# Performance work log

Measured on AMD Instinct MI355X. Metric: run time of the kernel, lower is better.

The kernel has to match this reference:

```python
import jax, jax.numpy as jnp
import numpy as np

M, NM, EM = 7, 1024, 32768        # modules, nodes/module, edges/module
N, E = M * NM, M * EM
F, D, H = 128, 64, 4              # node feats, hidden_channels, heads
HC = H * D


def setup_inputs() -> dict:
    key = jax.random.key(0)
    ks = jax.random.split(key, 20)
    x = jax.random.normal(ks[0], (N, F), jnp.float32)
    # intra-module edges; nodes of module m occupy [m*NM, (m+1)*NM)
    base = jnp.repeat(jnp.arange(M, dtype=jnp.int32) * NM, EM)
    src = base + jax.random.randint(ks[1], (E,), 0, NM, dtype=jnp.int32)
    dst = base + jax.random.randint(ks[2], (E,), 0, NM, dtype=jnp.int32)
    edge_index = jnp.stack([src, dst])
    module_assignments = jnp.repeat(jnp.arange(M, dtype=jnp.int32), NM)
    rn = lambda k, sh: jax.random.normal(k, sh, jnp.float32) * 0.05
    return dict(
        x=x, edge_index=edge_index, module_assignments=module_assignments,
        g1_w=rn(ks[3], (M, F, H, D)), g1_as=rn(ks[4], (M, H, D)), g1_ad=rn(ks[5], (M, H, D)),
        g1_b=jnp.zeros((M, HC), jnp.float32),
        g2_w=rn(ks[6], (M, HC, 1, D)), g2_as=rn(ks[7], (M, 1, D)), g2_ad=rn(ks[8], (M, 1, D)),
        g2_b=jnp.zeros((M, D), jnp.float32),
        sa_in_w=rn(ks[9], (M, 3 * D, D)), sa_in_b=jnp.zeros((M, 3 * D), jnp.float32),
        sa_out_w=rn(ks[10], (M, D, D)), sa_out_b=jnp.zeros((M, D), jnp.float32),
        ca_in_w=rn(ks[11], (3 * D, D)), ca_in_b=jnp.zeros((3 * D,), jnp.float32),
        ca_out_w=rn(ks[12], (D, D)), ca_out_b=jnp.zeros((D,), jnp.float32),
        fusion_w=jnp.ones((M,), jnp.float32) / M,
        fc_w=rn(ks[13], (M * D, D)), fc_b=jnp.zeros((D,), jnp.float32),
        c1_w=rn(ks[14], (D, D // 2)), c1_b=jnp.zeros((D // 2,), jnp.float32),
        c2_w=rn(ks[15], (D // 2, 2)), c2_b=jnp.zeros((2,), jnp.float32))


def _gat(x, src, dst, W, a_s, a_d, b, concat):
    # PyG-style GATConv (eval mode, add_self_loops=True). x:[NM,Fin], W:[Fin,h,c]
    h = jnp.einsum('nf,fhc->nhc', x, W)          # [NM,h,c]
    es = (h * a_s).sum(-1)                        # [NM,h]
    ed = (h * a_d).sum(-1)
    sl = jnp.arange(NM, dtype=src.dtype)
    s = jnp.concatenate([src, sl])                # add self-loops
    d = jnp.concatenate([dst, sl])
    e = jax.nn.leaky_relu(es[s] + ed[d], 0.2)     # [E+NM,h]
    mx = jax.ops.segment_max(e, d, num_segments=NM)
    ex = jnp.exp(e - mx[d])
    den = jax.ops.segment_sum(ex, d, num_segments=NM)
    alpha = ex / (den[d] + 1e-16)
    out = jax.ops.segment_sum(alpha[:, :, None] * h[s], d, num_segments=NM)  # [NM,h,c]
    out = out.reshape(NM, -1) if concat else out.mean(axis=1)
    return out + b


def _mha(x, in_w, in_b, out_w, out_b, nh):
    # torch nn.MultiheadAttention, batch_first, batch=1, eval mode
    L, d = x.shape
    dh = d // nh
    q, k, v = jnp.split(x @ in_w.T + in_b, 3, axis=-1)
    q = q.reshape(L, nh, dh); k = k.reshape(L, nh, dh); v = v.reshape(L, nh, dh)
    att = jax.nn.softmax(jnp.einsum('qhd,khd->hqk', q, k) * (1.0 / np.sqrt(dh)), axis=-1)
    o = jnp.einsum('hqk,khd->qhd', att, v).reshape(L, d)
    return o @ out_w.T + out_b


def _forward(x, edge_index, g1_w, g1_as, g1_ad, g1_b, g2_w, g2_as, g2_ad, g2_b,
             sa_in_w, sa_in_b, sa_out_w, sa_out_b, ca_in_w, ca_in_b, ca_out_w, ca_out_b,
             fusion_w, fc_w, fc_b, c1_w, c1_b, c2_w, c2_b):
    # per-module subgraph extraction + reindex: modules are contiguous node
    # blocks and edges are grouped per module, so mask/relabel is a reshape.
    ei = edge_index.reshape(2, M, EM)
    offs = (jnp.arange(M, dtype=ei.dtype) * NM)[:, None]
    src = ei[0] - offs                 # [M,EM] local indices
    dst = ei[1] - offs
    xm = x.reshape(M, NM, F)

    def per_module(xm_, s_, d_, g1w, g1a, g1d, g1b_, g2w_, g2a, g2d, g2b_, siw, sib, sow, sob):
        h = jax.nn.relu(_gat(xm_, s_, d_, g1w, g1a, g1d, g1b_, True))   # [NM,HC]
        h = jax.nn.relu(_gat(h, s_, d_, g2w_, g2a, g2d, g2b_, False))   # [NM,D]
        h = _mha(h, siw, sib, sow, sob, H)                              # module self-attention
        return h.mean(axis=0)                                            # [D]

    reps = jax.vmap(per_module)(xm, src, dst, g1_w, g1_as, g1_ad, g1_b,
                                g2_w, g2_as, g2_ad, g2_b,
                                sa_in_w, sa_in_b, sa_out_w, sa_out_b)    # [M,D]
    cross = _mha(reps, ca_in_w, ca_in_b, ca_out_w, ca_out_b, H)          # [M,D]
    w = jax.nn.softmax(fusion_w)
    fused = (cross * w[:, None]).reshape(1, M * D) @ fc_w + fc_b         # [1,D]
    out = jax.nn.relu(fused @ c1_w + c1_b) @ c2_w + c2_b                 # [1,2]
    return out, reps


def reference(x, edge_index, module_assignments, g1_w, g1_as, g1_ad, g1_b,
              g2_w, g2_as, g2_ad, g2_b, sa_in_w, sa_in_b, sa_out_w, sa_out_b,
              ca_in_w, ca_in_b, ca_out_w, ca_out_b, fusion_w, fc_w, fc_b,
              c1_w, c1_b, c2_w, c2_b):
    del module_assignments  # encoded as contiguous blocks of NM nodes per module
    return _forward(x, edge_index, g1_w, g1_as, g1_ad, g1_b, g2_w, g2_as, g2_ad, g2_b,
                    sa_in_w, sa_in_b, sa_out_w, sa_out_b, ca_in_w, ca_in_b, ca_out_w,
                    ca_out_b, fusion_w, fc_w, fc_b, c1_w, c1_b, c2_w, c2_b)
```

## Files before the change

### kernel.cpp

```cpp
#include <hip/hip_runtime.h>
#include <hip/hip_bf16.h>
#include <stdint.h>

#define MODS 7
#define NMOD 1024
#define EMOD 32768
#define NN (MODS*NMOD)
#define EE (MODS*EMOD)
#define KC2 4
#define G1B (MODS*16*4)

typedef __hip_bfloat16 bf16;

static __device__ __forceinline__ float lrelu(float x){ return x > 0.f ? x : 0.2f*x; }
static __device__ __forceinline__ float bfu(unsigned short u){ return __uint_as_float(((unsigned)u) << 16); }
static __device__ __forceinline__ float2 f2fma(float2 a, float2 b, float2 c){
  return make_float2(fmaf(a.x,b.x,c.x), fmaf(a.y,b.y,c.y));
}

template<int K, int JT, bool TB, int RT, bool OBF, int SC>
__device__ __forceinline__ void gemm_body(int b, const float* __restrict__ A,
    const float* __restrict__ B, const float* __restrict__ bias, void* __restrict__ Cv,
    const float* __restrict__ a_s, const float* __restrict__ a_d,
    float* __restrict__ es, float* __restrict__ ed) {
  constexpr int jt = JT/64;
  constexpr int rtiles = NMOD/RT;
  constexpr int RPT = RT/16;
  int ct = b % jt; b /= jt;
  int rt = b % rtiles; b /= rtiles;
  int m = b;
  int row0 = m*NMOD + rt*RT;
  int col0 = ct*64;
  __shared__ float Ast[32][RT+4];
  __shared__ float Bs[32][68];
  float acc[RPT][4] = {};
  int tid = threadIdx.x;
  int tr = (tid >> 4) * RPT;
  int tc = (tid & 15) * 4;
  const float* Bm = B + (size_t)m*K*JT;
  for (int k0 = 0; k0 < K; k0 += 32) {
    if constexpr (RT >= 32) {
      constexpr int ANUM = RT*32/1024;
      #pragma unroll
      for (int i = 0; i < ANUM; ++i) {
        int it = tid + i*256;
        int rr = it >> 3, kk0 = (it & 7)*4;
        float4 t = *(const float4*)&A[(size_t)(row0+rr)*K + k0 + kk0];
        Ast[kk0+0][rr] = t.x; Ast[kk0+1][rr] = t.y; Ast[kk0+2][rr] = t.z; Ast[kk0+3][rr] = t.w;
      }
    } else {
      if (tid < 128) {
        int rr = tid >> 3, kk0 = (tid & 7)*4;
        float4 t = *(const float4*)&A[(size_t)(row0+rr)*K + k0 + kk0];
        Ast[kk0+0][rr] = t.x; Ast[kk0+1][rr] = t.y; Ast[kk0+2][rr] = t.z; Ast[kk0+3][rr] = t.w;
      }
    }
    #pragma unroll
    for (int i = 0; i < 2; ++i) {
      int it = tid + i*256;
      if (!TB) {
        int kk = it >> 4, jj0 = (it & 15)*4;
        float4 t = *(const float4*)&Bm[(size_t)(k0+kk)*JT + col0 + jj0];
        Bs[kk][jj0] = t.x; Bs[kk][jj0+1] = t.y; Bs[kk][jj0+2] = t.z; Bs[kk][jj0+3] = t.w;
      } else {
        int jj = it >> 3, kk0 = (it & 7)*4;
        float4 t = *(const float4*)&Bm[(size_t)(col0+jj)*K + k0 + kk0];
        Bs[kk0+0][jj] = t.x; Bs[kk0+1][jj] = t.y; Bs[kk0+2][jj] = t.z; Bs[kk0+3][jj] = t.w;
      }
    }
    __syncthreads();
    #pragma unroll
    for (int kk = 0; kk < 32; ++kk) {
      float4 bv = *(const float4*)&Bs[kk][tc];
      float av[RPT];
      if constexpr (RPT == 4) {
        float4 t = *(const float4*)&Ast[kk][tr];
        av[0] = t.x; av[1] = t.y; av[2] = t.z; av[3] = t.w;
      } else if constexpr (RPT == 2) {
        av[0] = Ast[kk][tr]; av[1] = Ast[kk][tr+1];
      } else {
        av[0] = Ast[kk][tr];
      }
      #pragma unroll
      for (int i = 0; i < RPT; ++i) {
        acc[i][0] += av[i]*bv.x; acc[i][1] += av[i]*bv.y;
        acc[i][2] += av[i]*bv.z; acc[i][3] += av[i]*bv.w;
      }
    }
    __syncthreads();
  }
  float4 bb = {0,0,0,0};
  if (bias) bb = *(const float4*)&bias[m*JT + col0 + tc];
  #pragma unroll
  for (int i = 0; i < RPT; ++i) {
    float4 o = { acc[i][0]+bb.x, acc[i][1]+bb.y, acc[i][2]+bb.z, acc[i][3]+bb.w };
    size_t idx = (size_t)(row0+tr+i)*JT + col0 + tc;
    if constexpr (OBF) {
      bf16* Cp = (bf16*)Cv;
      bf16 tmp[4] = { __float2bfloat16(o.x), __float2bfloat16(o.y),
                      __float2bfloat16(o.z), __float2bfloat16(o.w) };
      *(uint2*)&Cp[idx] = *(const uint2*)tmp;
    } else {
      float* Cp = (float*)Cv;
      *(float4*)&Cp[idx] = o;
    }
  }
  if constexpr (SC == 4) {
    int hh = ct;
    float4 as4 = *(const float4*)&a_s[(m*4 + hh)*64 + tc];
    float4 ad4 = *(const float4*)&a_d[(m*4 + hh)*64 + tc];
    #pragma unroll
    for (int i = 0; i < RPT; ++i) {
      float s = acc[i][0]*as4.x + acc[i][1]*as4.y + acc[i][2]*as4.z + acc[i][3]*as4.w;
      float d = acc[i][0]*ad4.x + acc[i][1]*ad4.y + acc[i][2]*ad4.z + acc[i][3]*ad4.w;
      #pragma unroll
      for (int off = 1; off < 16; off <<= 1) { s += __shfl_xor(s, off); d += __shfl_xor(d, off); }
      if ((tid & 15) == 0) {
        es[(row0+tr+i)*4 + hh] = s;
        ed[(row0+tr+i)*4 + hh] = d;
      }
    }
  }
  if constexpr (SC == 1) {
    float4 as4 = *(const float4*)&a_s[m*64 + tc];
    float4 ad4 = *(const float4*)&a_d[m*64 + tc];
    float s = acc[0][0]*as4.x + acc[0][1]*as4.y + acc[0][2]*as4.z + acc[0][3]*as4.w;
    float d = acc[0][0]*ad4.x + acc[0][1]*ad4.y + acc[0][2]*ad4.z + acc[0][3]*ad4.w;
    #pragma unroll
    for (int off = 1; off < 16; off <<= 1) { s += __shfl_xor(s, off); d += __shfl_xor(d, off); }
    if ((tid & 15) == 0) { es[row0+tr] = s; ed[row0+tr] = d; }
  }
}

__device__ __forceinline__ void hist_body(int mm, const int* __restrict__ dst,
                                          int* __restrict__ rs, int* __restrict__ rs2) {
  __shared__ int hc[NMOD];
  __shared__ int hws[4];
  int tid = threadIdx.x;
  hc[tid] = 0; hc[tid+256] = 0; hc[tid+512] = 0; hc[tid+768] = 0;
  __syncthreads();
  const int4* d4 = (const int4*)(dst + mm*EMOD);
  int base = mm*NMOD;
  for (int it = tid; it < EMOD/4; it += 256) {
    int4 d = d4[it];
    atomicAdd(&hc[d.x - base], 1); atomicAdd(&hc[d.y - base], 1);
    atomicAdd(&hc[d.z - base], 1); atomicAdd(&hc[d.w - base], 1);
  }
  __syncthreads();
  int lane = tid & 63, wid = tid >> 6;
  int i0 = tid*4;
  int v0 = hc[i0], v1 = hc[i0+1], v2 = hc[i0+2], v3 = hc[i0+3];
  int T = v0+v1+v2+v3;
  int X = T;
  #pragma unroll
  for (int off = 1; off < 64; off <<= 1) { int t = __shfl_up(X, off); if (lane >= off) X += t; }
  if (lane == 63) hws[wid] = X;
  __syncthreads();
  int woff = 0;
  #pragma unroll
  for (int w = 0; w < 4; ++w) if (w < wid) woff += hws[w];
  int ex = mm*EMOD + woff + X - T;
  int4 o = make_int4(ex, ex+v0, ex+v0+v1, ex+v0+v1+v2);
  *(int4*)&rs[base + i0]  = o;
  *(int4*)&rs2[base + i0] = o;
  if (mm == MODS-1 && tid == 255) rs[NN] = EE;
}

__global__ __launch_bounds__(256) void k_g1h(const float* __restrict__ x,
    const float* __restrict__ g1w, bf16* __restrict__ h1,
    const float* __restrict__ a_s, const float* __restrict__ a_d,
    float* __restrict__ es, float* __restrict__ ed,
    const int* __restrict__ dst, int* __restrict__ rs, int* __restrict__ rs2) {
  if (blockIdx.x < G1B)
    gemm_body<128,256,false,64,true,4>(blockIdx.x, x, g1w, nullptr, h1, a_s, a_d, es, ed);
  else
    hist_body(blockIdx.x - G1B, dst, rs, rs2);
}

__global__ __launch_bounds__(256) void k_g2s(const float* __restrict__ A,
    const float* __restrict__ B, bf16* __restrict__ h2,
    const float* __restrict__ a_s, const float* __restrict__ a_d,
    float* __restrict__ es, float* __restrict__ ed) {
  gemm_body<256,64,false,16,true,1>(blockIdx.x, A, B, nullptr, h2, a_s, a_d, es, ed);
}

__global__ __launch_bounds__(256) void k_gqkv(const float* __restrict__ A,
    const float* __restrict__ B, const float* __restrict__ bias, float* __restrict__ C) {
  gemm_body<64,192,true,64,false,0>(blockIdx.x, A, B, bias, C, nullptr, nullptr, nullptr, nullptr);
}

__global__ void k_fill(const int* __restrict__ src, const int* __restrict__ dst,
                       int* __restrict__ rs2, int* __restrict__ csr_src) {
  int e = blockIdx.x*256 + threadIdx.x;
  if (e < EE) {
    int pos = atomicAdd(&rs2[dst[e]], 1);
    csr_src[pos] = src[e];
  }
}

__global__ __launch_bounds__(256) void k_agg4(const bf16* __restrict__ h,
    const float* __restrict__ es, const float* __restrict__ ed, const int* __restrict__ rs,
    const int* __restrict__ csr_src, const float* __restrict__ bias, float* __restrict__ out) {
  int wid = __builtin_amdgcn_readfirstlane(threadIdx.x >> 6);
  int n = blockIdx.x*4 + wid;
  int lane = threadIdx.x & 63;
  int hh = lane >> 4;
  int m = n >> 10;
  const unsigned short* hp = (const unsigned short*)h;
  float edv = ed[n*4 + hh];
  float p0 = __expf(lrelu(es[n*4 + hh] + edv));
  float den = p0;
  ushort4 v0 = *(const ushort4*)&hp[(size_t)n*256 + lane*4];
  float a0 = p0*bfu(v0.x), a1 = p0*bfu(v0.y), a2 = p0*bfu(v0.z), a3 = p0*bfu(v0.w);
  int beg = rs[n], end = rs[n+1];
  int i = beg;
  for (; i + 8 <= end; i += 8) {
    int ss[8]; ushort4 ww[8]; float qq[8];
    #pragma unroll
    for (int k = 0; k < 8; ++k) ss[k] = csr_src[i+k];
    #pragma unroll
    for (int k = 0; k < 8; ++k) ww[k] = *(const ushort4*)&hp[(size_t)ss[k]*256 + lane*4];
    #pragma unroll
    for (int k = 0; k < 8; ++k) qq[k] = __expf(lrelu(es[ss[k]*4 + hh] + edv));
    #pragma unroll
    for (int k = 0; k < 8; ++k) {
      den += qq[k];
      a0 += qq[k]*bfu(ww[k].x); a1 += qq[k]*bfu(ww[k].y);
      a2 += qq[k]*bfu(ww[k].z); a3 += qq[k]*bfu(ww[k].w);
    }
  }
  for (; i < end; ++i) {
    int s = csr_src[i];
    ushort4 w = *(const ushort4*)&hp[(size_t)s*256 + lane*4];
    float q = __expf(lrelu(es[s*4 + hh] + edv));
    den += q;
    a0 += q*bfu(w.x); a1 += q*bfu(w.y); a2 += q*bfu(w.z); a3 += q*bfu(w.w);
  }
  float inv = 1.f/den;
  float4 bb = *(const float4*)&bias[m*256 + lane*4];
  float4 o = { fmaxf(a0*inv + bb.x, 0.f), fmaxf(a1*inv + bb.y, 0.f),
               fmaxf(a2*inv + bb.z, 0.f), fmaxf(a3*inv + bb.w, 0.f) };
  *(float4*)&out[(size_t)n*256 + lane*4] = o;
}

__global__ __launch_bounds__(256) void k_agg1(const bf16* __restrict__ h,
    const float* __restrict__ es, const float* __restrict__ ed, const int* __restrict__ rs,
    const int* __restrict__ csr_src, const float* __restrict__ bias, float* __restrict__ out) {
  int wid = __builtin_amdgcn_readfirstlane(threadIdx.x >> 6);
  int n = blockIdx.x*4 + wid;
  int lane = threadIdx.x & 63;
  int m = n >> 10;
  float edv = ed[n];
  float p0 = __expf(lrelu(es[n] + edv));
  float den = p0;
  float acc = p0 * __bfloat162float(h[(size_t)n*64 + lane]);
  int beg = rs[n], end = rs[n+1];
  int i = beg;
  for (; i + 8 <= end; i += 8) {
    int ss[8]; float vv[8]; float qq[8];
    #pragma unroll
    for (int k = 0; k < 8; ++k) ss[k] = csr_src[i+k];
    #pragma unroll
    for (int k = 0; k < 8; ++k) vv[k] = __bfloat162float(h[(size_t)ss[k]*64 + lane]);
    #pragma unroll
    for (int k = 0; k < 8; ++k) qq[k] = __expf(lrelu(es[ss[k]] + edv));
    #pragma unroll
    for (int k = 0; k < 8; ++k) { den += qq[k]; acc += qq[k]*vv[k]; }
  }
  for (; i < end; ++i) {
    int s = csr_src[i];
    float q = __expf(lrelu(es[s] + edv));
    den += q;
    acc += q * __bfloat162float(h[(size_t)s*64 + lane]);
  }
  float v = acc/den + bias[m*64 + lane];
  out[(size_t)n*64 + lane] = fmaxf(v, 0.f);
}

__global__ __launch_bounds__(256) void k_attn(const float* __restrict__ qkv,
    float* __restrict__ pd, float* __restrict__ pacc) {
  int b = blockIdx.x;
  int kcg = b & (KC2-1); b /= KC2;
  int h = b & 3; b >>= 2;
  int qt = b & 15; int m = b >> 4;
  int lane = threadIdx.x & 63;
  int wu = __builtin_amdgcn_readfirstlane(threadIdx.x >> 6);
  int n = m*NMOD + qt*64 + lane;
  float2 q2[8];
  const float* qrow = qkv + (size_t)n*192 + h*16;
  #pragma unroll
  for (int c = 0; c < 8; ++c) {
    float2 t = *(const float2*)(qrow + 2*c);
    q2[c] = make_float2(t.x*0.25f, t.y*0.25f);
  }
  const float* kb = qkv + (size_t)(m*NMOD + kcg*256 + wu*64)*192 + 64 + h*16;
  float den = 0.f;
  float2 acc2[8] = {};
  float2 kreg[8];
  #pragma unroll
  for (int c = 0; c < 8; ++c) kreg[c] = ((const float2*)kb)[c];
  for (int j = 0; j < 64; ++j) {
    const float2* nk = (const float2*)(kb + (size_t)(j+1)*192);
    float2 knx[8];
    #pragma unroll
    for (int c = 0; c < 8; ++c) knx[c] = nk[c];
    float2 d0 = {0,0}, d1 = {0,0};
    #pragma unroll
    for (int c = 0; c < 8; c += 2) { d0 = f2fma(q2[c], kreg[c], d0); d1 = f2fma(q2[c+1], kreg[c+1], d1); }
    float p = __expf((d0.x + d0.y) + (d1.x + d1.y));
    den += p;
    const float2* vr2 = (const float2*)(kb + (size_t)j*192 + 64);
    float2 pp = {p, p};
    #pragma unroll
    for (int c = 0; c < 8; ++c) acc2[c] = f2fma(pp, vr2[c], acc2[c]);
    #pragma unroll
    for (int c = 0; c < 8; ++c) kreg[c] = knx[c];
  }
  __shared__ float red[4][64][17];
  #pragma unroll
  for (int c = 0; c < 8; ++c) { red[wu][lane][2*c] = acc2[c].x; red[wu][lane][2*c+1] = acc2[c].y; }
  red[wu][lane][16] = den;
  __syncthreads();
  if (wu == 0) {
    size_t o = ((size_t)n*4 + h)*KC2 + kcg;
    pd[o] = red[0][lane][16] + red[1][lane][16] + red[2][lane][16] + red[3][lane][16];
    #pragma unroll
    for (int c = 0; c < 16; ++c)
      pacc[o*16 + c] = red[0][lane][c] + red[1][lane][c] + red[2][lane][c] + red[3][lane][c];
  }
}

__global__ void k_attn_combine(const float* __restrict__ pd, const float* __restrict__ pacc,
                               float* __restrict__ attn) {
  int t = blockIdx.x*256 + threadIdx.x;
  if (t >= NN*4) return;
  float den = 0.f;
  #pragma unroll
  for (int kc = 0; kc < KC2; ++kc) den += pd[(size_t)t*KC2 + kc];
  float inv = 1.f/den;
  int n = t >> 2, h = t & 3;
  #pragma unroll
  for (int c = 0; c < 16; ++c) {
    float s = 0.f;
    #pragma unroll
    for (int kc = 0; kc < KC2; ++kc) s += pacc[((size_t)t*KC2 + kc)*16 + c];
    attn[(size_t)n*64 + h*16 + c] = s*inv;
  }
}

__global__ void k_reps(const float* __restrict__ attn, const float* __restrict__ out_w,
                       const float* __restrict__ out_b, float* __restrict__ reps,
                       float* __restrict__ dout) {
  int m = blockIdx.x;
  __shared__ float part[4][64];
  __shared__ float abar[64];
  int c = threadIdx.x & 63, pp = threadIdx.x >> 6;
  float s = 0.f;
  const float* base = attn + (size_t)m*NMOD*64;
  for (int i = pp*256; i < pp*256 + 256; ++i) s += base[(size_t)i*64 + c];
  part[pp][c] = s;
  __syncthreads();
  if (pp == 0) abar[c] = (part[0][c]+part[1][c]+part[2][c]+part[3][c]) * (1.f/NMOD);
  __syncthreads();
  if (threadIdx.x < 64) {
    int j = threadIdx.x;
    float r = out_b[m*64 + j];
    const float* wr = out_w + (size_t)m*64*64 + (size_t)j*64;
    #pragma unroll
    for (int k = 0; k < 64; ++k) r += abar[k]*wr[k];
    reps[m*64 + j] = r;
    dout[2 + m*64 + j] = r;
  }
}

__global__ __launch_bounds__(256) void k_final(const float* __restrict__ reps,
    const float* __restrict__ ca_in_w, const float* __restrict__ ca_in_b,
    const float* __restrict__ ca_out_w, const float* __restrict__ ca_out_b,
    const float* __restrict__ fusion_w, const float* __restrict__ fc_w,
    const float* __restrict__ fc_b, const float* __restrict__ c1_w,
    const float* __restrict__ c1_b, const float* __restrict__ c2_w,
    const float* __restrict__ c2_b, float* __restrict__ dout) {
  __shared__ float R[7][64];
  __shared__ float QKV[7][192];
  __shared__ float SC[4][7][8];
  __shared__ float AL[4][7][8];
  __shared__ float O[7][64];
  __shared__ float CR[7][64];
  __shared__ float W[8];
  __shared__ float part[4][64];
  __shared__ float FU[64];
  __shared__ float HM[32];
  int tid = threadIdx.x, lane = tid & 63;
  for (int i = tid; i < 448; i += 256) R[i>>6][i&63] = reps[i];
  __syncthreads();
  {
    int sub = tid & 3, tt0 = tid >> 2;
    #pragma unroll 3
    for (int it = 0; it < 21; ++it) {
      int t = tt0 + it*64;
      int r = t/192, j = t - r*192;
      const float4* wr = (const float4*)&ca_in_w[j*64 + sub*16];
      const float4* rr = (const float4*)&R[r][sub*16];
      float s = 0.f;
      #pragma unroll
      for (int c = 0; c < 4; ++c) {
        float4 a = rr[c], w4 = wr[c];
        s += a.x*w4.x + a.y*w4.y + a.z*w4.z + a.w*w4.w;
      }
      s += __shfl_xor(s, 1); s += __shfl_xor(s, 2);
      if (sub == 0) QKV[r][j] = s + ca_in_b[j];
    }
    if (tid == 252) {
      float p[7]; float den = 0.f;
      #pragma unroll
      for (int i = 0; i < 7; ++i) { p[i] = __expf(fusion_w[i]); den += p[i]; }
      float inv = 1.f/den;
      #pragma unroll
      for (int i = 0; i < 7; ++i) W[i] = p[i]*inv;
    }
  }
  __syncthreads();
  if (tid < 196) {
    int hh = tid/49, rem = tid - hh*49, qi = rem/7, ki = rem - qi*7;
    float s = 0.f;
    #pragma unroll
    for (int c = 0; c < 16; ++c) s += QKV[qi][hh*16 + c]*QKV[ki][64 + hh*16 + c];
    SC[hh][qi][ki] = __expf(s*0.25f);
  }
  __syncthreads();
  if (tid < 28) {
    int hh = tid/7, qi = tid - hh*7;
    float den = 0.f;
    #pragma unroll
    for (int k = 0; k < 7; ++k) den += SC[hh][qi][k];
    float inv = 1.f/den;
    #pragma unroll
    for (int k = 0; k < 7; ++k) AL[hh][qi][k] = SC[hh][qi][k]*inv;
  }
  __syncthreads();
  for (int i = tid; i < 448; i += 256) {
    int qi = i >> 6, j = i & 63, hh = j >> 4;
    float s = 0.f;
    #pragma unroll
    for (int k = 0; k < 7; ++k) s += AL[hh][qi][k]*QKV[k][128 + j];
    O[qi][j] = s;
  }
  __syncthreads();
  {
    int sub = tid & 3, tt0 = tid >> 2;
    #pragma unroll
    for (int it = 0; it < 7; ++it) {
      int t = tt0 + it*64;
      int qi = t >> 6, j = t & 63;
      const float4* wr = (const float4*)&ca_out_w[j*64 + sub*16];
      const float4* orow = (const float4*)&O[qi][sub*16];
      float s = 0.f;
      #pragma unroll
      for (int c = 0; c < 4; ++c) {
        float4 a = orow[c], w4 = wr[c];
        s += a.x*w4.x + a.y*w4.y + a.z*w4.z + a.w*w4.w;
      }
      s += __shfl_xor(s, 1); s += __shfl_xor(s, 2);
      if (sub == 0) CR[qi][j] = s + ca_out_b[j];
    }
  }
  __syncthreads();
  {
    int w = tid >> 6;
    float s = 0.f;
    #pragma unroll 4
    for (int i = w*112; i < w*112 + 112; ++i)
      s += CR[i>>6][i&63]*W[i>>6]*fc_w[(size_t)i*64 + lane];
    part[w][lane] = s;
  }
  __syncthreads();
  if (tid < 64) FU[tid] = part[0][tid] + part[1][tid] + part[2][tid] + part[3][tid] + fc_b[tid];
  __syncthreads();
  if (tid < 128) {
    int sub = tid & 3, j = tid >> 2;
    float s = 0.f;
    #pragma unroll
    for (int c = 0; c < 16; ++c) { int k = sub*16 + c; s += FU[k]*c1_w[k*32 + j]; }
    s += __shfl_xor(s, 1); s += __shfl_xor(s, 2);
    if (sub == 0) HM[j] = fmaxf(s + c1_b[j], 0.f);
  }
  __syncthreads();
  if (tid < 2) {
    float s = c2_b[tid];
    #pragma unroll
    for (int k = 0; k < 32; ++k) s += HM[k]*c2_w[k*2 + tid];
    dout[tid] = s;
  }
}

extern "C" void kernel_launch(void* const* d_in, const int* in_sizes, int n_in,
                              void* d_out, int out_size, void* d_ws, size_t ws_size,
                              hipStream_t stream) {
  (void)in_sizes; (void)n_in; (void)out_size; (void)ws_size;
  const float* x       = (const float*)d_in[0];
  const int*   ei      = (const int*)d_in[1];
  const float* g1_w    = (const float*)d_in[3];
  const float* g1_as   = (const float*)d_in[4];
  const float* g1_ad   = (const float*)d_in[5];
  const float* g1_b    = (const float*)d_in[6];
  const float* g2_w    = (const float*)d_in[7];
  const float* g2_as   = (const float*)d_in[8];
  const float* g2_ad   = (const float*)d_in[9];
  const float* g2_b    = (const float*)d_in[10];
  const float* sa_in_w = (const float*)d_in[11];
  const float* sa_in_b = (const float*)d_in[12];
  const float* sa_out_w= (const float*)d_in[13];
  const float* sa_out_b= (const float*)d_in[14];
  const float* ca_in_w = (const float*)d_in[15];
  const float* ca_in_b = (const float*)d_in[16];
  const float* ca_out_w= (const float*)d_in[17];
  const float* ca_out_b= (const float*)d_in[18];
  const float* fusion_w= (const float*)d_in[19];
  const float* fc_w    = (const float*)d_in[20];
  const float* fc_b    = (const float*)d_in[21];
  const float* c1_w    = (const float*)d_in[22];
  const float* c1_b    = (const float*)d_in[23];
  const float* c2_w    = (const float*)d_in[24];
  const float* c2_b    = (const float*)d_in[25];
  float* dout = (float*)d_out;

  const int* src = ei;
  const int* dst = ei + EE;

  char* p = (char*)d_ws;
  int* rs      = (int*)p; p += (size_t)(NN+4)*sizeof(int);
  int* rs2     = (int*)p; p += (size_t)(NN+4)*sizeof(int);
  int* csr_src = (int*)p; p += (size_t)EE*sizeof(int);
  p = (char*)(((uintptr_t)p + 255) & ~(uintptr_t)255);
  float* h1f  = (float*)p; p += (size_t)NN*256*4;
  float* es1  = (float*)p; p += (size_t)NN*4*4;
  float* ed1  = (float*)p; p += (size_t)NN*4*4;
  float* gat1 = (float*)p; p += (size_t)NN*256*4;
  float* h2f  = (float*)p; p += (size_t)NN*64*4;
  float* es2  = (float*)p; p += (size_t)NN*4;
  float* ed2  = (float*)p; p += (size_t)NN*4;
  float* z    = (float*)p; p += (size_t)NN*64*4;
  float* attn = (float*)p; p += (size_t)NN*64*4;
  float* reps = (float*)p; p += (size_t)MODS*64*4;
  bf16* h1    = (bf16*)h1f;
  bf16* h2    = (bf16*)h2f;
  float* qkv  = h1f;
  float* pacc = gat1;
  float* pd   = h2f;

  k_g1h<<<G1B + MODS, 256, 0, stream>>>(x, g1_w, h1, g1_as, g1_ad, es1, ed1, dst, rs, rs2);
  k_fill<<<(EE+255)/256, 256, 0, stream>>>(src, dst, rs2, csr_src);
  k_agg4<<<NN/4, 256, 0, stream>>>(h1, es1, ed1, rs, csr_src, g1_b, gat1);
  k_g2s<<<MODS*64, 256, 0, stream>>>(gat1, g2_w, h2, g2_as, g2_ad, es2, ed2);
  k_agg1<<<NN/4, 256, 0, stream>>>(h2, es2, ed2, rs, csr_src, g2_b, z);
  k_gqkv<<<MODS*16*3, 256, 0, stream>>>(z, sa_in_w, sa_in_b, qkv);
  k_attn<<<MODS*16*4*KC2, 256, 0, stream>>>(qkv, pd, pacc);
  k_attn_combine<<<(NN*4+255)/256, 256, 0, stream>>>(pd, pacc, attn);
  k_reps<<<MODS, 256, 0, stream>>>(attn, sa_out_w, sa_out_b, reps, dout);
  k_final<<<1, 256, 0, stream>>>(reps, ca_in_w, ca_in_b, ca_out_w, ca_out_b,
                                 fusion_w, fc_w, fc_b, c1_w, c1_b, c2_w, c2_b, dout);
}
```

Measured before the change: 146.0 us.

## Store QKV planar per module and fuse attention combine into reps reduction

The QKV GEMM now writes Q, K and V into separate per-module planes, so the attention kernel streams contiguous K/V rows with a smaller stride. The separate attention-combine kernel is removed. Its normalisation and partial-sum merge are folded into the per-module mean reduction, which avoids writing and re-reading the attn buffer and drops one launch. The cost is that the fused reduction reads all partial accumulators through only seven blocks, which concentrates more memory traffic on very few CUs.

```diff
diff --git a/kernel.cpp b/kernel.cpp
--- a/kernel.cpp
+++ b/kernel.cpp
@@ -18,7 +18,7 @@
   return make_float2(fmaf(a.x,b.x,c.x), fmaf(a.y,b.y,c.y));
 }
 
-template<int K, int JT, bool TB, int RT, bool OBF, int SC>
+template<int K, int JT, bool TB, int RT, bool OBF, int SC, bool TRQ>
 __device__ __forceinline__ void gemm_body(int b, const float* __restrict__ A,
     const float* __restrict__ B, const float* __restrict__ bias, void* __restrict__ Cv,
     const float* __restrict__ a_s, const float* __restrict__ a_d,
@@ -94,15 +94,21 @@
   #pragma unroll
   for (int i = 0; i < RPT; ++i) {
     float4 o = { acc[i][0]+bb.x, acc[i][1]+bb.y, acc[i][2]+bb.z, acc[i][3]+bb.w };
-    size_t idx = (size_t)(row0+tr+i)*JT + col0 + tc;
-    if constexpr (OBF) {
-      bf16* Cp = (bf16*)Cv;
-      bf16 tmp[4] = { __float2bfloat16(o.x), __float2bfloat16(o.y),
-                      __float2bfloat16(o.z), __float2bfloat16(o.w) };
-      *(uint2*)&Cp[idx] = *(const uint2*)tmp;
+    if constexpr (TRQ) {
+      float* Cp = (float*)Cv;
+      size_t idx = ((size_t)(m*3 + ct)*NMOD + (rt*RT + tr + i))*64 + tc;
+      *(float4*)&Cp[idx] = o;
     } else {
-      float* Cp = (float*)Cv;
-      *(float4*)&Cp[idx] = o;
+      size_t idx = (size_t)(row0+tr+i)*JT + col0 + tc;
+      if constexpr (OBF) {
+        bf16* Cp = (bf16*)Cv;
+        bf16 tmp[4] = { __float2bfloat16(o.x), __float2bfloat16(o.y),
+                        __float2bfloat16(o.z), __float2bfloat16(o.w) };
+        *(uint2*)&Cp[idx] = *(const uint2*)tmp;
+      } else {
+        float* Cp = (float*)Cv;
+        *(float4*)&Cp[idx] = o;
+      }
     }
   }
   if constexpr (SC == 4) {
@@ -172,7 +178,7 @@
     float* __restrict__ es, float* __restrict__ ed,
     const int* __restrict__ dst, int* __restrict__ rs, int* __restrict__ rs2) {
   if (blockIdx.x < G1B)
-    gemm_body<128,256,false,64,true,4>(blockIdx.x, x, g1w, nullptr, h1, a_s, a_d, es, ed);
+    gemm_body<128,256,false,64,true,4,false>(blockIdx.x, x, g1w, nullptr, h1, a_s, a_d, es, ed);
   else
     hist_body(blockIdx.x - G1B, dst, rs, rs2);
 }
@@ -181,12 +187,12 @@
     const float* __restrict__ B, bf16* __restrict__ h2,
     const float* __restrict__ a_s, const float* __restrict__ a_d,
     float* __restrict__ es, float* __restrict__ ed) {
-  gemm_body<256,64,false,16,true,1>(blockIdx.x, A, B, nullptr, h2, a_s, a_d, es, ed);
+  gemm_body<256,64,false,16,true,1,false>(blockIdx.x, A, B, nullptr, h2, a_s, a_d, es, ed);
 }
 
 __global__ __launch_bounds__(256) void k_gqkv(const float* __restrict__ A,
     const float* __restrict__ B, const float* __restrict__ bias, float* __restrict__ C) {
-  gemm_body<64,192,true,64,false,0>(blockIdx.x, A, B, bias, C, nullptr, nullptr, nullptr, nullptr);
+  gemm_body<64,192,true,64,false,0,true>(blockIdx.x, A, B, bias, C, nullptr, nullptr, nullptr, nullptr);
 }
 
 __global__ void k_fill(const int* __restrict__ src, const int* __restrict__ dst,
@@ -285,22 +291,25 @@
   int qt = b & 15; int m = b >> 4;
   int lane = threadIdx.x & 63;
   int wu = __builtin_amdgcn_readfirstlane(threadIdx.x >> 6);
-  int n = m*NMOD + qt*64 + lane;
+  int nl = qt*64 + lane;
+  int n = m*NMOD + nl;
   float2 q2[8];
-  const float* qrow = qkv + (size_t)n*192 + h*16;
+  const float* qrow = qkv + ((size_t)(m*3 + 0)*NMOD + nl)*64 + h*16;
   #pragma unroll
   for (int c = 0; c < 8; ++c) {
     float2 t = *(const float2*)(qrow + 2*c);
     q2[c] = make_float2(t.x*0.25f, t.y*0.25f);
   }
-  const float* kb = qkv + (size_t)(m*NMOD + kcg*256 + wu*64)*192 + 64 + h*16;
+  int k0 = kcg*256 + wu*64;
+  const float* kb = qkv + ((size_t)(m*3 + 1)*NMOD + k0)*64 + h*16;
+  const float* vb = qkv + ((size_t)(m*3 + 2)*NMOD + k0)*64 + h*16;
   float den = 0.f;
   float2 acc2[8] = {};
   float2 kreg[8];
   #pragma unroll
   for (int c = 0; c < 8; ++c) kreg[c] = ((const float2*)kb)[c];
   for (int j = 0; j < 64; ++j) {
-    const float2* nk = (const float2*)(kb + (size_t)(j+1)*192);
+    const float2* nk = (const float2*)(kb + (size_t)(j+1)*64);
     float2 knx[8];
     #pragma unroll
     for (int c = 0; c < 8; ++c) knx[c] = nk[c];
@@ -309,7 +318,7 @@
     for (int c = 0; c < 8; c += 2) { d0 = f2fma(q2[c], kreg[c], d0); d1 = f2fma(q2[c+1], kreg[c+1], d1); }
     float p = __expf((d0.x + d0.y) + (d1.x + d1.y));
     den += p;
-    const float2* vr2 = (const float2*)(kb + (size_t)j*192 + 64);
+    const float2* vr2 = (const float2*)(vb + (size_t)j*64);
     float2 pp = {p, p};
     #pragma unroll
     for (int c = 0; c < 8; ++c) acc2[c] = f2fma(pp, vr2[c], acc2[c]);
@@ -330,46 +339,34 @@
   }
 }
 
-__global__ void k_attn_combine(const float* __restrict__ pd, const float* __restrict__ pacc,
-                               float* __restrict__ attn) {
-  int t = blockIdx.x*256 + threadIdx.x;
-  if (t >= NN*4) return;
-  float den = 0.f;
-  #pragma unroll
-  for (int kc = 0; kc < KC2; ++kc) den += pd[(size_t)t*KC2 + kc];
-  float inv = 1.f/den;
-  int n = t >> 2, h = t & 3;
-  #pragma unroll
-  for (int c = 0; c < 16; ++c) {
-    float s = 0.f;
-    #pragma unroll
-    for (int kc = 0; kc < KC2; ++kc) s += pacc[((size_t)t*KC2 + kc)*16 + c];
-    attn[(size_t)n*64 + h*16 + c] = s*inv;
-  }
-}
-
-__global__ void k_reps(const float* __restrict__ attn, const float* __restrict__ out_w,
-                       const float* __restrict__ out_b, float* __restrict__ reps,
-                       float* __restrict__ dout) {
+__global__ __launch_bounds__(256) void k_creps(const float* __restrict__ pd,
+    const float* __restrict__ pacc, const float* __restrict__ out_w,
+    const float* __restrict__ out_b, float* __restrict__ reps, float* __restrict__ dout) {
   int m = blockIdx.x;
   __shared__ float part[4][64];
   __shared__ float abar[64];
-  int c = threadIdx.x & 63, pp = threadIdx.x >> 6;
+  int tid = threadIdx.x;
+  int j = tid & 63, pp = tid >> 6;
+  int h = j >> 4, c = j & 15;
   float s = 0.f;
-  const float* base = attn + (size_t)m*NMOD*64;
-  for (int i = pp*256; i < pp*256 + 256; ++i) s += base[(size_t)i*64 + c];
-  part[pp][c] = s;
-  __syncthreads();
-  if (pp == 0) abar[c] = (part[0][c]+part[1][c]+part[2][c]+part[3][c]) * (1.f/NMOD);
-  __syncthreads();
-  if (threadIdx.x < 64) {
-    int j = threadIdx.x;
-    float r = out_b[m*64 + j];
-    const float* wr = out_w + (size_t)m*64*64 + (size_t)j*64;
+  for (int i = pp*256; i < pp*256 + 256; ++i) {
+    int n = m*NMOD + i;
+    size_t o = ((size_t)n*4 + h)*KC2;
+    float den = pd[o] + pd[o+1] + pd[o+2] + pd[o+3];
+    float t = pacc[o*16 + c] + pacc[(o+1)*16 + c] + pacc[(o+2)*16 + c] + pacc[(o+3)*16 + c];
+    s += t/den;
+  }
+  part[pp][j] = s;
+  __syncthreads();
+  if (pp == 0) abar[j] = (part[0][j]+part[1][j]+part[2][j]+part[3][j]) * (1.f/NMOD);
+  __syncthreads();
+  if (tid < 64) {
+    float r = out_b[m*64 + tid];
+    const float* wr = out_w + (size_t)m*64*64 + (size_t)tid*64;
     #pragma unroll
     for (int k = 0; k < 64; ++k) r += abar[k]*wr[k];
-    reps[m*64 + j] = r;
-    dout[2 + m*64 + j] = r;
+    reps[m*64 + tid] = r;
+    dout[2 + m*64 + tid] = r;
   }
 }
 
@@ -540,7 +537,6 @@
   float* es2  = (float*)p; p += (size_t)NN*4;
   float* ed2  = (float*)p; p += (size_t)NN*4;
   float* z    = (float*)p; p += (size_t)NN*64*4;
-  float* attn = (float*)p; p += (size_t)NN*64*4;
   float* reps = (float*)p; p += (size_t)MODS*64*4;
   bf16* h1    = (bf16*)h1f;
   bf16* h2    = (bf16*)h2f;
@@ -555,8 +551,7 @@
   k_agg1<<<NN/4, 256, 0, stream>>>(h2, es2, ed2, rs, csr_src, g2_b, z);
   k_gqkv<<<MODS*16*3, 256, 0, stream>>>(z, sa_in_w, sa_in_b, qkv);
   k_attn<<<MODS*16*4*KC2, 256, 0, stream>>>(qkv, pd, pacc);
-  k_attn_combine<<<(NN*4+255)/256, 256, 0, stream>>>(pd, pacc, attn);
-  k_reps<<<MODS, 256, 0, stream>>>(attn, sa_out_w, sa_out_b, reps, dout);
+  k_creps<<<MODS, 256, 0, stream>>>(pd, pacc, sa_out_w, sa_out_b, reps, dout);
   k_final<<<1, 256, 0, stream>>>(reps, ca_in_w, ca_in_b, ca_out_w, ca_out_b,
                                  fusion_w, fc_w, fc_b, c1_w, c1_b, c2_w, c2_b, dout);
 }
```

New measurement: 185.8 us. 1.27x slower.
